# Performance work log

Hardware: AMD Instinct MI355X
Metric: run time of the kernel (lower is better)

Reference implementation:

```python
import jax, jax.numpy as jnp
import numpy as np

B, N, DIM, T, H, DH = 4, 2048, 512, 16, 8, 64
EPS = 1e-5


def setup_inputs() -> dict:
    key = jax.random.key(0)
    ks = jax.random.split(key, 7)
    x = jax.random.normal(ks[0], (B, N, DIM), dtype=jnp.float32)
    # time-distance matrix, e.g. months between scans, in [0, 24)
    R = jax.random.uniform(ks[1], (B, T, T), dtype=jnp.float32) * 24.0
    gamma = jnp.ones((DIM,), dtype=jnp.float32)
    beta = jnp.zeros((DIM,), dtype=jnp.float32)
    W_qkv = jax.random.normal(ks[2], (DIM, 3 * H * DH), dtype=jnp.float32) * 0.02
    W_out = jax.random.normal(ks[3], (H * DH, DIM), dtype=jnp.float32) * 0.02
    a = jax.random.uniform(ks[4], (H,), dtype=jnp.float32)          # torch.rand(heads)
    c = 12.0 * jax.random.uniform(ks[5], (H,), dtype=jnp.float32)   # 12 * torch.rand(heads)
    return {"x": x, "R": R, "gamma": gamma, "beta": beta,
            "W_qkv": W_qkv, "W_out": W_out, "a": a, "c": c}


def reference(x, R, gamma, beta, W_qkv, W_out, a, c):
    b, n, dim = x.shape
    t = R.shape[-1]
    num_patches = n // t
    scale = DH ** -0.5

    # LayerNorm
    mu = jnp.mean(x, axis=-1, keepdims=True)
    var = jnp.mean(jnp.square(x - mu), axis=-1, keepdims=True)
    xn = (x - mu) * jax.lax.rsqrt(var + EPS) * gamma + beta

    # QKV projection -> [b, h, n, d]
    qkv = xn @ W_qkv  # [b, n, 3*h*d]
    q, k, v = jnp.split(qkv, 3, axis=-1)
    def to_heads(z):
        return z.reshape(b, n, H, DH).transpose(0, 2, 1, 3)
    q, k, v = to_heads(q), to_heads(k), to_heads(v)

    # attention scores with ReLU then learned sigmoid time-decay mask
    dots = jnp.einsum('bhnd,bhmd->bhnm', q, k) * scale
    dots = jax.nn.relu(dots)

    # flipped-sigmoid decay: 1 / (1 + exp(|a|*R - |c|)), per head  -> [b, h, t, t]
    decay = 1.0 / (1.0 + jnp.exp(jnp.abs(a)[None, :, None, None] * R[:, None, :, :]
                                 - jnp.abs(c)[None, :, None, None]))
    # expand timepoint mask to token resolution (repeat_interleave on both axes)
    decay = jnp.repeat(jnp.repeat(decay, num_patches, axis=2), num_patches, axis=3)

    attn = jax.nn.softmax(dots * decay, axis=-1)
    out = jnp.einsum('bhnm,bhmd->bhnd', attn, v)
    out = out.transpose(0, 2, 1, 3).reshape(b, n, H * DH)
    return out @ W_out  # dropout is identity at eval
```

## Files before the change

### kernel.cpp

```cpp
#include <hip/hip_runtime.h>
#include <math.h>

#define B_   4
#define N_   2048
#define DIM_ 512
#define T_   16
#define H_   8
#define DH_  64

typedef unsigned short ushort_t;
typedef __attribute__((ext_vector_type(8))) short bf16x8;
typedef __attribute__((ext_vector_type(16))) float f32x16;

__device__ inline ushort_t bf16_rn(float x) {
  unsigned u = __builtin_bit_cast(unsigned, x);
  u += 0x7FFFu + ((u >> 16) & 1u);
  return (ushort_t)(u >> 16);
}
__device__ inline float bf16f(ushort_t h) {
  return __builtin_bit_cast(float, (unsigned)h << 16);
}
__device__ inline unsigned pack2(ushort_t a, ushort_t b) {
  return (unsigned)a | ((unsigned)b << 16);
}
__device__ inline void split2(float x, ushort_t &h, ushort_t &l) {
  h = bf16_rn(x);
  l = bf16_rn(x - bf16f(h));
}
__device__ inline unsigned cvt_pk_bf16(float lo, float hi) {
  unsigned r;
  asm("v_cvt_pk_bf16_f32 %0, %1, %2" : "=v"(r) : "v"(lo), "v"(hi));
  return r;
}
__device__ inline void permlane32_swap(unsigned &x, unsigned &y) {
  asm volatile("v_permlane32_swap_b32 %0, %1" : "+v"(x), "+v"(y));
}
__device__ inline void gload_lds16(const ushort_t* g, ushort_t* l) {
  __builtin_amdgcn_global_load_lds(
      (const __attribute__((address_space(1))) unsigned int*)(g),
      (__attribute__((address_space(3))) unsigned int*)(l),
      16, 0, 0);
}

__global__ __launch_bounds__(256) void prep_kernel(
    const float* __restrict__ x, const float* __restrict__ gamma,
    const float* __restrict__ beta, const float* __restrict__ Wqkv,
    const float* __restrict__ Wout,
    ushort_t* __restrict__ xnh, ushort_t* __restrict__ xnl,
    ushort_t* __restrict__ wqh, ushort_t* __restrict__ wql,
    ushort_t* __restrict__ woh, ushort_t* __restrict__ wol) {
  __shared__ float Ts[64][68];
  int bidx = blockIdx.x;
  int tid = threadIdx.x;
  if (bidx < 256) {
    const float* src; ushort_t* dh; ushort_t* dl; int Nn, n0, k0;
    if (bidx < 192) {
      src = Wqkv; dh = wqh; dl = wql; Nn = 1536;
      n0 = (bidx % 24) * 64; k0 = (bidx / 24) * 64;
    } else {
      int l = bidx - 192;
      src = Wout; dh = woh; dl = wol; Nn = 512;
      n0 = (l % 8) * 64; k0 = (l / 8) * 64;
    }
#pragma unroll
    for (int it = 0; it < 4; ++it) {
      int idx = tid + it * 256;
      int r = idx >> 4, c4 = (idx & 15) * 4;
      *(float4*)&Ts[r][c4] = *(const float4*)&src[(size_t)(k0 + r) * Nn + n0 + c4];
    }
    __syncthreads();
#pragma unroll
    for (int it = 0; it < 2; ++it) {
      int idx = tid + it * 256;
      int n = idx >> 3, kc = (idx & 7) * 8;
      ushort_t hs[8], ls[8];
#pragma unroll
      for (int j = 0; j < 8; ++j) split2(Ts[kc + j][n], hs[j], ls[j]);
      uint4 uh, ul;
      uh.x = pack2(hs[0], hs[1]); uh.y = pack2(hs[2], hs[3]);
      uh.z = pack2(hs[4], hs[5]); uh.w = pack2(hs[6], hs[7]);
      ul.x = pack2(ls[0], ls[1]); ul.y = pack2(ls[2], ls[3]);
      ul.z = pack2(ls[4], ls[5]); ul.w = pack2(ls[6], ls[7]);
      size_t o = (size_t)(n0 + n) * 512 + k0 + kc;
      *(uint4*)&dh[o] = uh;
      *(uint4*)&dl[o] = ul;
    }
  } else {
    int row  = (bidx - 256) * 4 + (tid >> 6);
    int lane = tid & 63;
    const float4* xr = (const float4*)(x + (size_t)row * DIM_);
    float4 v0 = xr[lane * 2 + 0];
    float4 v1 = xr[lane * 2 + 1];
    float s  = v0.x + v0.y + v0.z + v0.w + v1.x + v1.y + v1.z + v1.w;
    float ss = v0.x*v0.x + v0.y*v0.y + v0.z*v0.z + v0.w*v0.w
             + v1.x*v1.x + v1.y*v1.y + v1.z*v1.z + v1.w*v1.w;
#pragma unroll
    for (int off = 32; off > 0; off >>= 1) {
      s  += __shfl_xor(s, off);
      ss += __shfl_xor(ss, off);
    }
    float mu  = s * (1.0f / DIM_);
    float var = ss * (1.0f / DIM_) - mu * mu;
    float rstd = rsqrtf(var + 1e-5f);
    float4 g0 = *(const float4*)&gamma[lane * 8];
    float4 g1 = *(const float4*)&gamma[lane * 8 + 4];
    float4 b0 = *(const float4*)&beta[lane * 8];
    float4 b1 = *(const float4*)&beta[lane * 8 + 4];
    float xv[8] = {v0.x, v0.y, v0.z, v0.w, v1.x, v1.y, v1.z, v1.w};
    float gv[8] = {g0.x, g0.y, g0.z, g0.w, g1.x, g1.y, g1.z, g1.w};
    float bv[8] = {b0.x, b0.y, b0.z, b0.w, b1.x, b1.y, b1.z, b1.w};
    ushort_t hs[8], ls[8];
#pragma unroll
    for (int j = 0; j < 8; ++j) {
      float xn = (xv[j] - mu) * rstd * gv[j] + bv[j];
      split2(xn, hs[j], ls[j]);
    }
    uint4 uh, ul;
    uh.x = pack2(hs[0], hs[1]); uh.y = pack2(hs[2], hs[3]);
    uh.z = pack2(hs[4], hs[5]); uh.w = pack2(hs[6], hs[7]);
    ul.x = pack2(ls[0], ls[1]); ul.y = pack2(ls[2], ls[3]);
    ul.z = pack2(ls[4], ls[5]); ul.w = pack2(ls[6], ls[7]);
    size_t o = (size_t)row * DIM_ + lane * 8;
    *(uint4*)&xnh[o] = uh;
    *(uint4*)&xnl[o] = ul;
  }
}

__global__ __launch_bounds__(256) void qkv_gemm_mfma(
    const ushort_t* __restrict__ xnh, const ushort_t* __restrict__ xnl,
    const ushort_t* __restrict__ wth, const ushort_t* __restrict__ wtl,
    ushort_t* __restrict__ qh, ushort_t* __restrict__ ql,
    ushort_t* __restrict__ kho, ushort_t* __restrict__ klo,
    ushort_t* __restrict__ vt) {
  __shared__ ushort_t Ah[128 * 40], Al[128 * 40], Bh[128 * 40], Bl[128 * 40];
  int tid = threadIdx.x;
  int w = tid >> 6, lane = tid & 63, l31 = lane & 31, g = lane >> 5;
  int wm = w >> 1, wn = w & 1;
  int idx = blockIdx.x;
  int xcd = idx & 7, local = idx >> 3;
  int n0 = (local % 12) * 128;
  int m0 = ((local / 12) * 8 + xcd) * 128;

  f32x16 acc[2][2];
#pragma unroll
  for (int i = 0; i < 2; ++i)
#pragma unroll
    for (int j = 0; j < 2; ++j)
#pragma unroll
      for (int e = 0; e < 16; ++e) acc[i][j][e] = 0.0f;

  int fm[2], fc[2];
#pragma unroll
  for (int it = 0; it < 2; ++it) {
    int f = tid + it * 256;
    fm[it] = f >> 2;
    fc[it] = (f & 3) * 8;
  }

#pragma unroll 1
  for (int kt = 0; kt < 16; ++kt) {
    __syncthreads();
#pragma unroll
    for (int it = 0; it < 2; ++it) {
      size_t ao = (size_t)(m0 + fm[it]) * 512 + kt * 32 + fc[it];
      size_t bo = (size_t)(n0 + fm[it]) * 512 + kt * 32 + fc[it];
      uint4 tah = *(const uint4*)&xnh[ao];
      uint4 tal = *(const uint4*)&xnl[ao];
      uint4 tbh = *(const uint4*)&wth[bo];
      uint4 tbl = *(const uint4*)&wtl[bo];
      int o = fm[it] * 40 + fc[it];
      *(uint4*)&Ah[o] = tah;
      *(uint4*)&Al[o] = tal;
      *(uint4*)&Bh[o] = tbh;
      *(uint4*)&Bl[o] = tbl;
    }
    __syncthreads();
#pragma unroll
    for (int kc = 0; kc < 2; ++kc) {
      int off = kc * 16 + 8 * g;
      bf16x8 afh[2], afl[2], bfh[2], bfl[2];
#pragma unroll
      for (int rb = 0; rb < 2; ++rb) {
        int r = (wm * 64 + rb * 32 + l31) * 40 + off;
        afh[rb] = *(const bf16x8*)&Ah[r];
        afl[rb] = *(const bf16x8*)&Al[r];
      }
#pragma unroll
      for (int cb = 0; cb < 2; ++cb) {
        int r = (wn * 64 + cb * 32 + l31) * 40 + off;
        bfh[cb] = *(const bf16x8*)&Bh[r];
        bfl[cb] = *(const bf16x8*)&Bl[r];
      }
#pragma unroll
      for (int rb = 0; rb < 2; ++rb)
#pragma unroll
        for (int cb = 0; cb < 2; ++cb) {
          acc[rb][cb] = __builtin_amdgcn_mfma_f32_32x32x16_bf16(afh[rb], bfh[cb], acc[rb][cb], 0, 0, 0);
          acc[rb][cb] = __builtin_amdgcn_mfma_f32_32x32x16_bf16(afh[rb], bfl[cb], acc[rb][cb], 0, 0, 0);
          acc[rb][cb] = __builtin_amdgcn_mfma_f32_32x32x16_bf16(afl[rb], bfh[cb], acc[rb][cb], 0, 0, 0);
        }
    }
  }

  int part = n0 >> 9;
#pragma unroll
  for (int rb = 0; rb < 2; ++rb) {
    int m_base = m0 + wm * 64 + rb * 32;
#pragma unroll
    for (int cb = 0; cb < 2; ++cb) {
      int n_g = n0 + wn * 64 + cb * 32 + l31;
      int rem = n_g & 511, hh = rem >> 6, d = rem & 63;
      if (part == 2) {
#pragma unroll
        for (int grp = 0; grp < 4; ++grp) {
          int m_g = m_base + grp * 8 + 4 * g;
          int bb = m_g >> 11, tok = m_g & 2047;
          uint2 pk;
          pk.x = pack2(bf16_rn(acc[rb][cb][grp * 4 + 0]), bf16_rn(acc[rb][cb][grp * 4 + 1]));
          pk.y = pack2(bf16_rn(acc[rb][cb][grp * 4 + 2]), bf16_rn(acc[rb][cb][grp * 4 + 3]));
          *(uint2*)&vt[((size_t)(bb * 8 + hh) * 64 + d) * 2048 + tok] = pk;
        }
      } else {
        float sc = (part == 0) ? 0.125f : 1.0f;
        ushort_t* dsth = (part == 0) ? qh : kho;
        ushort_t* dstl = (part == 0) ? ql : klo;
#pragma unroll
        for (int reg = 0; reg < 16; ++reg) {
          int row = (reg & 3) + 8 * (reg >> 2) + 4 * g;
          int m_g = m_base + row;
          int bb = m_g >> 11, tok = m_g & 2047;
          ushort_t hi, lo;
          split2(acc[rb][cb][reg] * sc, hi, lo);
          size_t addr = ((size_t)(bb * 8 + hh) * 2048 + tok) * 64 + d;
          dsth[addr] = hi;
          dstl[addr] = lo;
        }
      }
    }
  }
}

__global__ __launch_bounds__(256, 2) void attn_mfma(
    const ushort_t* __restrict__ qh, const ushort_t* __restrict__ ql,
    const ushort_t* __restrict__ kho, const ushort_t* __restrict__ klo,
    const ushort_t* __restrict__ vt, const float* __restrict__ R,
    const float* __restrict__ a, const float* __restrict__ c,
    ushort_t* __restrict__ aoh, ushort_t* __restrict__ aol) {
  __shared__ __align__(16) ushort_t KhS[2 * 4608];
  __shared__ __align__(16) ushort_t KlS[2 * 4608];
  __shared__ __align__(16) ushort_t VtS[2 * 4608];
  __shared__ float rsS[128];
  __shared__ float decl2S[16];

  int tid = threadIdx.x;
  int w = tid >> 6, lane = tid & 63, l31 = lane & 31, g = lane >> 5;
  int bh = blockIdx.x;
  int qt = blockIdx.y;
  int b = bh >> 3, h = bh & 7;

  int qrow = qt * 128 + w * 32 + l31;
  size_t qoff = ((size_t)bh * 2048 + qrow) * 64;
  bf16x8 qfh[4], qfl[4];
#pragma unroll
  for (int d0i = 0; d0i < 4; ++d0i) {
    qfh[d0i] = *(const bf16x8*)&qh[qoff + d0i * 16 + 8 * g];
    qfl[d0i] = *(const bf16x8*)&ql[qoff + d0i * 16 + 8 * g];
  }

  const ushort_t* kbase = kho + (size_t)bh * 2048 * 64;
  const ushort_t* lbase = klo + (size_t)bh * 2048 * 64;
  const ushort_t* vbase = vt + (size_t)bh * 64 * 2048;

  if (tid < 16) {
    float aab = fabsf(a[h]);
    float cab = fabsf(c[h]);
    float Rv = R[b * (T_ * T_) + qt * T_ + tid];
    decl2S[tid] = 1.4426950408889634f / (1.0f + __expf(aab * Rv - cab));
  }

  int r_[3], j8_[3];
#pragma unroll
  for (int i = 0; i < 3; ++i) {
    int ch = (i < 2) ? (w + i * 4) : 8;
    int u = ch * 512 + lane * 8;
    int r = u / 72;
    int j = (u - r * 72) >> 3;
    r_[i] = r;
    j8_[i] = (j == 8) ? 0 : (j << 3);
  }
  int a8 = (w < 3) ? w : 0;

  f32x16 oacc[2];
#pragma unroll
  for (int t = 0; t < 2; ++t)
#pragma unroll
    for (int i = 0; i < 16; ++i) oacc[t][i] = 0.0f;
  float rsp[4] = {0.0f, 0.0f, 0.0f, 0.0f};

  {
#pragma unroll
    for (int i = 0; i < 2; ++i) {
      int cb = (w + i * 4) * 512;
      gload_lds16(&kbase[(size_t)r_[i] * 64 + j8_[i]], &KhS[cb]);
      gload_lds16(&lbase[(size_t)r_[i] * 64 + j8_[i]], &KlS[cb]);
      gload_lds16(&vbase[(size_t)r_[i] * 2048 + j8_[i]], &VtS[cb]);
    }
    int cb8 = 8 * 512;
    if (a8 == 0)      gload_lds16(&kbase[(size_t)r_[2] * 64 + j8_[2]], &KhS[cb8]);
    else if (a8 == 1) gload_lds16(&lbase[(size_t)r_[2] * 64 + j8_[2]], &KlS[cb8]);
    else              gload_lds16(&vbase[(size_t)r_[2] * 2048 + j8_[2]], &VtS[cb8]);
  }
  __syncthreads();

  int cur = 0;

#pragma unroll 1
  for (int kt = 0; kt < 32; ++kt) {
    int kb = cur * 4608;

    float decl2 = decl2S[kt >> 1];
    bf16x8 kfh[2][4], kfl[2][4], vf[2][4];
#pragma unroll
    for (int khalf = 0; khalf < 2; ++khalf) {
      int krow = kb + (khalf * 32 + l31) * 72;
#pragma unroll
      for (int d0i = 0; d0i < 4; ++d0i) {
        int off = krow + d0i * 16 + 8 * g;
        kfh[khalf][d0i] = *(const bf16x8*)&KhS[off];
        kfl[khalf][d0i] = *(const bf16x8*)&KlS[off];
      }
    }
#pragma unroll
    for (int dt = 0; dt < 2; ++dt) {
      int vrow = kb + (dt * 32 + l31) * 72;
#pragma unroll
      for (int kc = 0; kc < 4; ++kc)
        vf[dt][kc] = *(const bf16x8*)&VtS[vrow + kc * 16 + 8 * g];
    }
    __builtin_amdgcn_sched_barrier(0);

    if (kt + 1 < 32) {
      int lb = (cur ^ 1) * 4608;
      int kk = kt + 1;
#pragma unroll
      for (int i = 0; i < 2; ++i) {
        int cb = lb + (w + i * 4) * 512;
        gload_lds16(&kbase[(size_t)kk * 4096 + r_[i] * 64 + j8_[i]], &KhS[cb]);
        gload_lds16(&lbase[(size_t)kk * 4096 + r_[i] * 64 + j8_[i]], &KlS[cb]);
        gload_lds16(&vbase[(size_t)r_[i] * 2048 + kk * 64 + j8_[i]], &VtS[cb]);
      }
      int cb8 = lb + 8 * 512;
      if (a8 == 0)      gload_lds16(&kbase[(size_t)kk * 4096 + r_[2] * 64 + j8_[2]], &KhS[cb8]);
      else if (a8 == 1) gload_lds16(&lbase[(size_t)kk * 4096 + r_[2] * 64 + j8_[2]], &KlS[cb8]);
      else              gload_lds16(&vbase[(size_t)r_[2] * 2048 + kk * 64 + j8_[2]], &VtS[cb8]);
    }
    __builtin_amdgcn_sched_barrier(0);

    bf16x8 pa[4];
#pragma unroll
    for (int khalf = 0; khalf < 2; ++khalf) {
      f32x16 sacc;
#pragma unroll
      for (int i = 0; i < 16; ++i) sacc[i] = 0.0f;
#pragma unroll
      for (int d0i = 0; d0i < 4; ++d0i) {
        sacc = __builtin_amdgcn_mfma_f32_32x32x16_bf16(kfh[khalf][d0i], qfh[d0i], sacc, 0, 0, 0);
        sacc = __builtin_amdgcn_mfma_f32_32x32x16_bf16(kfl[khalf][d0i], qfh[d0i], sacc, 0, 0, 0);
        sacc = __builtin_amdgcn_mfma_f32_32x32x16_bf16(kfh[khalf][d0i], qfl[d0i], sacc, 0, 0, 0);
      }
#pragma unroll
      for (int reg = 0; reg < 16; ++reg) {
        float pvv = exp2f(fmaxf(sacc[reg], 0.0f) * decl2);
        rsp[reg & 3] += pvv;
        sacc[reg] = pvv;
      }
#pragma unroll
      for (int hf = 0; hf < 2; ++hf) {
        unsigned d0 = cvt_pk_bf16(sacc[hf * 8 + 0], sacc[hf * 8 + 1]);
        unsigned d1 = cvt_pk_bf16(sacc[hf * 8 + 2], sacc[hf * 8 + 3]);
        unsigned d2 = cvt_pk_bf16(sacc[hf * 8 + 4], sacc[hf * 8 + 5]);
        unsigned d3 = cvt_pk_bf16(sacc[hf * 8 + 6], sacc[hf * 8 + 7]);
        permlane32_swap(d0, d2);
        permlane32_swap(d1, d3);
        uint4 u; u.x = d0; u.y = d1; u.z = d2; u.w = d3;
        pa[khalf * 2 + hf] = __builtin_bit_cast(bf16x8, u);
      }
    }

#pragma unroll
    for (int dt = 0; dt < 2; ++dt)
#pragma unroll
      for (int kc = 0; kc < 4; ++kc)
        oacc[dt] = __builtin_amdgcn_mfma_f32_32x32x16_bf16(pa[kc], vf[dt][kc], oacc[dt], 0, 0, 0);

    __builtin_amdgcn_s_barrier();
    cur ^= 1;
  }

  float rs = (rsp[0] + rsp[1]) + (rsp[2] + rsp[3]);
  rs += __shfl_xor(rs, 32);
  rsS[w * 32 + l31] = rs;

#pragma unroll
  for (int reg = 0; reg < 16; ++reg) {
    int row = (reg & 3) + 8 * (reg >> 2) + 4 * g;
    float invs = 1.0f / rsS[w * 32 + row];
    int tok = qt * 128 + w * 32 + row;
#pragma unroll
    for (int dt = 0; dt < 2; ++dt) {
      int d = dt * 32 + l31;
      ushort_t hi, lo;
      split2(oacc[dt][reg] * invs, hi, lo);
      size_t addr = ((size_t)b * 2048 + tok) * 512 + h * 64 + d;
      aoh[addr] = hi;
      aol[addr] = lo;
    }
  }
}

__global__ __launch_bounds__(256) void out_gemm_mfma(
    const ushort_t* __restrict__ ah, const ushort_t* __restrict__ al,
    const ushort_t* __restrict__ wth, const ushort_t* __restrict__ wtl,
    float* __restrict__ out) {
  __shared__ ushort_t Ah[128 * 40], Al[128 * 40], Bh[128 * 40], Bl[128 * 40];
  int tid = threadIdx.x;
  int w = tid >> 6, lane = tid & 63, l31 = lane & 31, g = lane >> 5;
  int wm = w >> 1, wn = w & 1;
  int idx = blockIdx.x;
  int xcd = idx & 7, local = idx >> 3;
  int n0 = (local & 3) * 128;
  int m0 = ((local >> 2) * 8 + xcd) * 128;

  f32x16 acc[2][2];
#pragma unroll
  for (int i = 0; i < 2; ++i)
#pragma unroll
    for (int j = 0; j < 2; ++j)
#pragma unroll
      for (int e = 0; e < 16; ++e) acc[i][j][e] = 0.0f;

  int fm[2], fc[2];
#pragma unroll
  for (int it = 0; it < 2; ++it) {
    int f = tid + it * 256;
    fm[it] = f >> 2;
    fc[it] = (f & 3) * 8;
  }

#pragma unroll 1
  for (int kt = 0; kt < 16; ++kt) {
    __syncthreads();
#pragma unroll
    for (int it = 0; it < 2; ++it) {
      size_t ao = (size_t)(m0 + fm[it]) * 512 + kt * 32 + fc[it];
      size_t bo = (size_t)(n0 + fm[it]) * 512 + kt * 32 + fc[it];
      uint4 tah = *(const uint4*)&ah[ao];
      uint4 tal = *(const uint4*)&al[ao];
      uint4 tbh = *(const uint4*)&wth[bo];
      uint4 tbl = *(const uint4*)&wtl[bo];
      int o = fm[it] * 40 + fc[it];
      *(uint4*)&Ah[o] = tah;
      *(uint4*)&Al[o] = tal;
      *(uint4*)&Bh[o] = tbh;
      *(uint4*)&Bl[o] = tbl;
    }
    __syncthreads();
#pragma unroll
    for (int kc = 0; kc < 2; ++kc) {
      int off = kc * 16 + 8 * g;
      bf16x8 afh[2], afl[2], bfh[2], bfl[2];
#pragma unroll
      for (int rb = 0; rb < 2; ++rb) {
        int r = (wm * 64 + rb * 32 + l31) * 40 + off;
        afh[rb] = *(const bf16x8*)&Ah[r];
        afl[rb] = *(const bf16x8*)&Al[r];
      }
#pragma unroll
      for (int cb = 0; cb < 2; ++cb) {
        int r = (wn * 64 + cb * 32 + l31) * 40 + off;
        bfh[cb] = *(const bf16x8*)&Bh[r];
        bfl[cb] = *(const bf16x8*)&Bl[r];
      }
#pragma unroll
      for (int rb = 0; rb < 2; ++rb)
#pragma unroll
        for (int cb = 0; cb < 2; ++cb) {
          acc[rb][cb] = __builtin_amdgcn_mfma_f32_32x32x16_bf16(afh[rb], bfh[cb], acc[rb][cb], 0, 0, 0);
          acc[rb][cb] = __builtin_amdgcn_mfma_f32_32x32x16_bf16(afh[rb], bfl[cb], acc[rb][cb], 0, 0, 0);
          acc[rb][cb] = __builtin_amdgcn_mfma_f32_32x32x16_bf16(afl[rb], bfh[cb], acc[rb][cb], 0, 0, 0);
        }
    }
  }

#pragma unroll
  for (int rb = 0; rb < 2; ++rb) {
    int m_base = m0 + wm * 64 + rb * 32;
#pragma unroll
    for (int cb = 0; cb < 2; ++cb) {
      int n_g = n0 + wn * 64 + cb * 32 + l31;
#pragma unroll
      for (int reg = 0; reg < 16; ++reg) {
        int row = (reg & 3) + 8 * (reg >> 2) + 4 * g;
        out[(size_t)(m_base + row) * 512 + n_g] = acc[rb][cb][reg];
      }
    }
  }
}

extern "C" void kernel_launch(void* const* d_in, const int* in_sizes, int n_in,
                              void* d_out, int out_size, void* d_ws, size_t ws_size,
                              hipStream_t stream) {
  (void)in_sizes; (void)n_in;
  const float* x     = (const float*)d_in[0];
  const float* R     = (const float*)d_in[1];
  const float* gamma = (const float*)d_in[2];
  const float* beta  = (const float*)d_in[3];
  const float* Wqkv  = (const float*)d_in[4];
  const float* Wout  = (const float*)d_in[5];
  const float* av    = (const float*)d_in[6];
  const float* cv    = (const float*)d_in[7];
  float* out = (float*)d_out;

  const size_t EL  = (size_t)B_ * N_ * DIM_;
  const size_t SZT = EL * sizeof(ushort_t);

  char* p = (char*)d_ws;
  ushort_t* wqh = (ushort_t*)p;                  p += (size_t)1536 * 512 * 2;
  ushort_t* wql = (ushort_t*)p;                  p += (size_t)1536 * 512 * 2;
  ushort_t* woh = (ushort_t*)p;                  p += (size_t)512 * 512 * 2;
  ushort_t* wol = (ushort_t*)p;                  p += (size_t)512 * 512 * 2;
  ushort_t* qhb = (ushort_t*)p;                  p += SZT;
  ushort_t* qlb = (ushort_t*)p;                  p += SZT;
  ushort_t* khb = (ushort_t*)p;                  p += SZT;
  ushort_t* klb = (ushort_t*)p;                  p += SZT;
  ushort_t* vtb = (ushort_t*)p;                  p += SZT;
  size_t base_need = (size_t)(p - (char*)d_ws);
  size_t needA = base_need + 2 * SZT;

  bool planA = (ws_size >= needA);
  ushort_t* xnh = planA ? (ushort_t*)p : (ushort_t*)d_out;
  ushort_t* xnl = xnh + EL;
  float* gemm_dst = planA ? out : (float*)qhb;

  prep_kernel<<<dim3(2304), dim3(256), 0, stream>>>(x, gamma, beta, Wqkv, Wout,
                                                    xnh, xnl, wqh, wql, woh, wol);
  qkv_gemm_mfma<<<dim3(768), dim3(256), 0, stream>>>(xnh, xnl, wqh, wql,
                                                     qhb, qlb, khb, klb, vtb);
  attn_mfma<<<dim3(32, 16), dim3(256), 0, stream>>>(qhb, qlb, khb, klb, vtb,
                                                    R, av, cv, xnh, xnl);
  out_gemm_mfma<<<dim3(256), dim3(256), 0, stream>>>(xnh, xnl, woh, wol, gemm_dst);
  if (!planA) {
    hipMemcpyAsync(out, gemm_dst, (size_t)out_size * sizeof(float),
                   hipMemcpyDeviceToDevice, stream);
  }
}
```

Measured before the change: 235.6 us.

## Shrink attention blocks to two waves with single-buffered LDS and priority hints

The attention kernel now uses 128-thread blocks covering 64 query rows, doubling the grid, and single-buffers the K/Kl/Vt tiles in LDS instead of double-buffering them. This cuts LDS per block so more blocks can be resident. The price is that each K/V tile is reloaded by twice as many blocks, and the loop needs extra waits and barriers, which removes the load/compute overlap within a block. It also raises wave priority around the MFMA sections and replaces exp2f with raw v_exp_f32 to cut softmax instruction overhead.

```diff
diff --git a/kernel.cpp b/kernel.cpp
--- a/kernel.cpp
+++ b/kernel.cpp
@@ -34,6 +34,11 @@
 }
 __device__ inline void permlane32_swap(unsigned &x, unsigned &y) {
   asm volatile("v_permlane32_swap_b32 %0, %1" : "+v"(x), "+v"(y));
+}
+__device__ inline float exp2_raw(float x) {
+  float r;
+  asm("v_exp_f32 %0, %1" : "=v"(r) : "v"(x));
+  return r;
 }
 __device__ inline void gload_lds16(const ushort_t* g, ushort_t* l) {
   __builtin_amdgcn_global_load_lds(
@@ -240,16 +245,16 @@
   }
 }
 
-__global__ __launch_bounds__(256, 2) void attn_mfma(
+__global__ __launch_bounds__(128, 2) void attn_mfma(
     const ushort_t* __restrict__ qh, const ushort_t* __restrict__ ql,
     const ushort_t* __restrict__ kho, const ushort_t* __restrict__ klo,
     const ushort_t* __restrict__ vt, const float* __restrict__ R,
     const float* __restrict__ a, const float* __restrict__ c,
     ushort_t* __restrict__ aoh, ushort_t* __restrict__ aol) {
-  __shared__ __align__(16) ushort_t KhS[2 * 4608];
-  __shared__ __align__(16) ushort_t KlS[2 * 4608];
-  __shared__ __align__(16) ushort_t VtS[2 * 4608];
-  __shared__ float rsS[128];
+  __shared__ __align__(16) ushort_t KhS[4608];
+  __shared__ __align__(16) ushort_t KlS[4608];
+  __shared__ __align__(16) ushort_t VtS[4608];
+  __shared__ float rsS[64];
   __shared__ float decl2S[16];
 
   int tid = threadIdx.x;
@@ -258,7 +263,7 @@
   int qt = blockIdx.y;
   int b = bh >> 3, h = bh & 7;
 
-  int qrow = qt * 128 + w * 32 + l31;
+  int qrow = qt * 64 + w * 32 + l31;
   size_t qoff = ((size_t)bh * 2048 + qrow) * 64;
   bf16x8 qfh[4], qfl[4];
 #pragma unroll
@@ -274,21 +279,23 @@
   if (tid < 16) {
     float aab = fabsf(a[h]);
     float cab = fabsf(c[h]);
-    float Rv = R[b * (T_ * T_) + qt * T_ + tid];
+    float Rv = R[b * (T_ * T_) + (qt >> 1) * T_ + tid];
     decl2S[tid] = 1.4426950408889634f / (1.0f + __expf(aab * Rv - cab));
   }
 
-  int r_[3], j8_[3];
-#pragma unroll
-  for (int i = 0; i < 3; ++i) {
-    int ch = (i < 2) ? (w + i * 4) : 8;
-    int u = ch * 512 + lane * 8;
+  int r_[4], j8_[4];
+#pragma unroll
+  for (int i = 0; i < 4; ++i) {
+    int u = (w * 4 + i) * 512 + lane * 8;
     int r = u / 72;
     int j = (u - r * 72) >> 3;
     r_[i] = r;
     j8_[i] = (j == 8) ? 0 : (j << 3);
   }
-  int a8 = (w < 3) ? w : 0;
+  int u8 = 8 * 512 + lane * 8;
+  int r8 = u8 / 72;
+  int j8v = (u8 - r8 * 72) >> 3;
+  int j88 = (j8v == 8) ? 0 : (j8v << 3);
 
   f32x16 oacc[2];
 #pragma unroll
@@ -299,30 +306,28 @@
 
   {
 #pragma unroll
-    for (int i = 0; i < 2; ++i) {
-      int cb = (w + i * 4) * 512;
+    for (int i = 0; i < 4; ++i) {
+      int cb = (w * 4 + i) * 512;
       gload_lds16(&kbase[(size_t)r_[i] * 64 + j8_[i]], &KhS[cb]);
       gload_lds16(&lbase[(size_t)r_[i] * 64 + j8_[i]], &KlS[cb]);
       gload_lds16(&vbase[(size_t)r_[i] * 2048 + j8_[i]], &VtS[cb]);
     }
-    int cb8 = 8 * 512;
-    if (a8 == 0)      gload_lds16(&kbase[(size_t)r_[2] * 64 + j8_[2]], &KhS[cb8]);
-    else if (a8 == 1) gload_lds16(&lbase[(size_t)r_[2] * 64 + j8_[2]], &KlS[cb8]);
-    else              gload_lds16(&vbase[(size_t)r_[2] * 2048 + j8_[2]], &VtS[cb8]);
+    if (w == 0) {
+      gload_lds16(&kbase[(size_t)r8 * 64 + j88], &KhS[8 * 512]);
+      gload_lds16(&lbase[(size_t)r8 * 64 + j88], &KlS[8 * 512]);
+    } else {
+      gload_lds16(&vbase[(size_t)r8 * 2048 + j88], &VtS[8 * 512]);
+    }
   }
   __syncthreads();
-
-  int cur = 0;
 
 #pragma unroll 1
   for (int kt = 0; kt < 32; ++kt) {
-    int kb = cur * 4608;
-
     float decl2 = decl2S[kt >> 1];
     bf16x8 kfh[2][4], kfl[2][4], vf[2][4];
 #pragma unroll
     for (int khalf = 0; khalf < 2; ++khalf) {
-      int krow = kb + (khalf * 32 + l31) * 72;
+      int krow = (khalf * 32 + l31) * 72;
 #pragma unroll
       for (int d0i = 0; d0i < 4; ++d0i) {
         int off = krow + d0i * 16 + 8 * g;
@@ -332,27 +337,30 @@
     }
 #pragma unroll
     for (int dt = 0; dt < 2; ++dt) {
-      int vrow = kb + (dt * 32 + l31) * 72;
+      int vrow = (dt * 32 + l31) * 72;
 #pragma unroll
       for (int kc = 0; kc < 4; ++kc)
         vf[dt][kc] = *(const bf16x8*)&VtS[vrow + kc * 16 + 8 * g];
     }
+    asm volatile("s_waitcnt lgkmcnt(0)" ::: "memory");
     __builtin_amdgcn_sched_barrier(0);
+    __builtin_amdgcn_s_barrier();
 
     if (kt + 1 < 32) {
-      int lb = (cur ^ 1) * 4608;
       int kk = kt + 1;
 #pragma unroll
-      for (int i = 0; i < 2; ++i) {
-        int cb = lb + (w + i * 4) * 512;
+      for (int i = 0; i < 4; ++i) {
+        int cb = (w * 4 + i) * 512;
         gload_lds16(&kbase[(size_t)kk * 4096 + r_[i] * 64 + j8_[i]], &KhS[cb]);
         gload_lds16(&lbase[(size_t)kk * 4096 + r_[i] * 64 + j8_[i]], &KlS[cb]);
         gload_lds16(&vbase[(size_t)r_[i] * 2048 + kk * 64 + j8_[i]], &VtS[cb]);
       }
-      int cb8 = lb + 8 * 512;
-      if (a8 == 0)      gload_lds16(&kbase[(size_t)kk * 4096 + r_[2] * 64 + j8_[2]], &KhS[cb8]);
-      else if (a8 == 1) gload_lds16(&lbase[(size_t)kk * 4096 + r_[2] * 64 + j8_[2]], &KlS[cb8]);
-      else              gload_lds16(&vbase[(size_t)r_[2] * 2048 + kk * 64 + j8_[2]], &VtS[cb8]);
+      if (w == 0) {
+        gload_lds16(&kbase[(size_t)kk * 4096 + r8 * 64 + j88], &KhS[8 * 512]);
+        gload_lds16(&lbase[(size_t)kk * 4096 + r8 * 64 + j88], &KlS[8 * 512]);
+      } else {
+        gload_lds16(&vbase[(size_t)r8 * 2048 + kk * 64 + j88], &VtS[8 * 512]);
+      }
     }
     __builtin_amdgcn_sched_barrier(0);
 
@@ -362,15 +370,17 @@
       f32x16 sacc;
 #pragma unroll
       for (int i = 0; i < 16; ++i) sacc[i] = 0.0f;
+      __builtin_amdgcn_s_setprio(1);
 #pragma unroll
       for (int d0i = 0; d0i < 4; ++d0i) {
         sacc = __builtin_amdgcn_mfma_f32_32x32x16_bf16(kfh[khalf][d0i], qfh[d0i], sacc, 0, 0, 0);
         sacc = __builtin_amdgcn_mfma_f32_32x32x16_bf16(kfl[khalf][d0i], qfh[d0i], sacc, 0, 0, 0);
         sacc = __builtin_amdgcn_mfma_f32_32x32x16_bf16(kfh[khalf][d0i], qfl[d0i], sacc, 0, 0, 0);
       }
+      __builtin_amdgcn_s_setprio(0);
 #pragma unroll
       for (int reg = 0; reg < 16; ++reg) {
-        float pvv = exp2f(fmaxf(sacc[reg], 0.0f) * decl2);
+        float pvv = exp2_raw(fmaxf(sacc[reg], 0.0f) * decl2);
         rsp[reg & 3] += pvv;
         sacc[reg] = pvv;
       }
@@ -387,14 +397,16 @@
       }
     }
 
+    __builtin_amdgcn_s_setprio(1);
 #pragma unroll
     for (int dt = 0; dt < 2; ++dt)
 #pragma unroll
       for (int kc = 0; kc < 4; ++kc)
         oacc[dt] = __builtin_amdgcn_mfma_f32_32x32x16_bf16(pa[kc], vf[dt][kc], oacc[dt], 0, 0, 0);
-
+    __builtin_amdgcn_s_setprio(0);
+
+    asm volatile("s_waitcnt vmcnt(0)" ::: "memory");
     __builtin_amdgcn_s_barrier();
-    cur ^= 1;
   }
 
   float rs = (rsp[0] + rsp[1]) + (rsp[2] + rsp[3]);
@@ -405,7 +417,7 @@
   for (int reg = 0; reg < 16; ++reg) {
     int row = (reg & 3) + 8 * (reg >> 2) + 4 * g;
     float invs = 1.0f / rsS[w * 32 + row];
-    int tok = qt * 128 + w * 32 + row;
+    int tok = qt * 64 + w * 32 + row;
 #pragma unroll
     for (int dt = 0; dt < 2; ++dt) {
       int d = dt * 32 + l31;
@@ -546,7 +558,7 @@
                                                     xnh, xnl, wqh, wql, woh, wol);
   qkv_gemm_mfma<<<dim3(768), dim3(256), 0, stream>>>(xnh, xnl, wqh, wql,
                                                      qhb, qlb, khb, klb, vtb);
-  attn_mfma<<<dim3(32, 16), dim3(256), 0, stream>>>(qhb, qlb, khb, klb, vtb,
+  attn_mfma<<<dim3(32, 32), dim3(128), 0, stream>>>(qhb, qlb, khb, klb, vtb,
                                                     R, av, cv, xnh, xnl);
   out_gemm_mfma<<<dim3(256), dim3(256), 0, stream>>>(xnh, xnl, woh, wol, gemm_dst);
   if (!planA) {
```

Result: slower. 241.6 us (+2.6%).

## Load GEMM tiles via direct global-to-LDS loads, use raw v_exp in attention

Applied to the files above, without the earlier changes.

Both projection GEMMs now stage their tiles with global_load_lds instead of register round-trips. Each wave fills one of the four hi/lo operand tiles, and the padding column is filled with a duplicate chunk so the padded 40-element row stride is kept. The attention softmax uses the raw v_exp_f32 instruction instead of exp2f, which avoids range-handling code. An explicit vmcnt(0) wait is added before the attention loop barrier to order the async LDS loads. The aim is to save VGPR traffic and instructions in tile staging. The cost is that only one wave issues loads per tile and the waits are coarse.

```diff
diff --git a/kernel.cpp b/kernel.cpp
--- a/kernel.cpp
+++ b/kernel.cpp
@@ -34,6 +34,11 @@
 }
 __device__ inline void permlane32_swap(unsigned &x, unsigned &y) {
   asm volatile("v_permlane32_swap_b32 %0, %1" : "+v"(x), "+v"(y));
+}
+__device__ inline float exp2_raw(float x) {
+  float r;
+  asm("v_exp_f32 %0, %1" : "=v"(r) : "v"(x));
+  return r;
 }
 __device__ inline void gload_lds16(const ushort_t* g, ushort_t* l) {
   __builtin_amdgcn_global_load_lds(
@@ -132,7 +137,10 @@
     ushort_t* __restrict__ qh, ushort_t* __restrict__ ql,
     ushort_t* __restrict__ kho, ushort_t* __restrict__ klo,
     ushort_t* __restrict__ vt) {
-  __shared__ ushort_t Ah[128 * 40], Al[128 * 40], Bh[128 * 40], Bl[128 * 40];
+  __shared__ __align__(16) ushort_t Ah[128 * 40];
+  __shared__ __align__(16) ushort_t Al[128 * 40];
+  __shared__ __align__(16) ushort_t Bh[128 * 40];
+  __shared__ __align__(16) ushort_t Bl[128 * 40];
   int tid = threadIdx.x;
   int w = tid >> 6, lane = tid & 63, l31 = lane & 31, g = lane >> 5;
   int wm = w >> 1, wn = w & 1;
@@ -149,30 +157,35 @@
 #pragma unroll
       for (int e = 0; e < 16; ++e) acc[i][j][e] = 0.0f;
 
-  int fm[2], fc[2];
-#pragma unroll
-  for (int it = 0; it < 2; ++it) {
-    int f = tid + it * 256;
-    fm[it] = f >> 2;
-    fc[it] = (f & 3) * 8;
+  int rowbase = (w < 2) ? m0 : n0;
+  int off_[10];
+#pragma unroll
+  for (int ci = 0; ci < 10; ++ci) {
+    int u = ci * 512 + lane * 8;
+    int r = u / 40;
+    int j = (u - r * 40) >> 3;
+    off_[ci] = (rowbase + r) * 512 + ((j == 4) ? 0 : (j << 3));
   }
 
 #pragma unroll 1
   for (int kt = 0; kt < 16; ++kt) {
     __syncthreads();
-#pragma unroll
-    for (int it = 0; it < 2; ++it) {
-      size_t ao = (size_t)(m0 + fm[it]) * 512 + kt * 32 + fc[it];
-      size_t bo = (size_t)(n0 + fm[it]) * 512 + kt * 32 + fc[it];
-      uint4 tah = *(const uint4*)&xnh[ao];
-      uint4 tal = *(const uint4*)&xnl[ao];
-      uint4 tbh = *(const uint4*)&wth[bo];
-      uint4 tbl = *(const uint4*)&wtl[bo];
-      int o = fm[it] * 40 + fc[it];
-      *(uint4*)&Ah[o] = tah;
-      *(uint4*)&Al[o] = tal;
-      *(uint4*)&Bh[o] = tbh;
-      *(uint4*)&Bl[o] = tbl;
+    if (w == 0) {
+#pragma unroll
+      for (int ci = 0; ci < 10; ++ci)
+        gload_lds16(&xnh[(size_t)off_[ci] + kt * 32], &Ah[ci * 512]);
+    } else if (w == 1) {
+#pragma unroll
+      for (int ci = 0; ci < 10; ++ci)
+        gload_lds16(&xnl[(size_t)off_[ci] + kt * 32], &Al[ci * 512]);
+    } else if (w == 2) {
+#pragma unroll
+      for (int ci = 0; ci < 10; ++ci)
+        gload_lds16(&wth[(size_t)off_[ci] + kt * 32], &Bh[ci * 512]);
+    } else {
+#pragma unroll
+      for (int ci = 0; ci < 10; ++ci)
+        gload_lds16(&wtl[(size_t)off_[ci] + kt * 32], &Bl[ci * 512]);
     }
     __syncthreads();
 #pragma unroll
@@ -370,7 +383,7 @@
       }
 #pragma unroll
       for (int reg = 0; reg < 16; ++reg) {
-        float pvv = exp2f(fmaxf(sacc[reg], 0.0f) * decl2);
+        float pvv = exp2_raw(fmaxf(sacc[reg], 0.0f) * decl2);
         rsp[reg & 3] += pvv;
         sacc[reg] = pvv;
       }
@@ -393,6 +406,7 @@
       for (int kc = 0; kc < 4; ++kc)
         oacc[dt] = __builtin_amdgcn_mfma_f32_32x32x16_bf16(pa[kc], vf[dt][kc], oacc[dt], 0, 0, 0);
 
+    asm volatile("s_waitcnt vmcnt(0)" ::: "memory");
     __builtin_amdgcn_s_barrier();
     cur ^= 1;
   }
@@ -422,7 +436,10 @@
     const ushort_t* __restrict__ ah, const ushort_t* __restrict__ al,
     const ushort_t* __restrict__ wth, const ushort_t* __restrict__ wtl,
     float* __restrict__ out) {
-  __shared__ ushort_t Ah[128 * 40], Al[128 * 40], Bh[128 * 40], Bl[128 * 40];
+  __shared__ __align__(16) ushort_t Ah[128 * 40];
+  __shared__ __align__(16) ushort_t Al[128 * 40];
+  __shared__ __align__(16) ushort_t Bh[128 * 40];
+  __shared__ __align__(16) ushort_t Bl[128 * 40];
   int tid = threadIdx.x;
   int w = tid >> 6, lane = tid & 63, l31 = lane & 31, g = lane >> 5;
   int wm = w >> 1, wn = w & 1;
@@ -439,30 +456,35 @@
 #pragma unroll
       for (int e = 0; e < 16; ++e) acc[i][j][e] = 0.0f;
 
-  int fm[2], fc[2];
-#pragma unroll
-  for (int it = 0; it < 2; ++it) {
-    int f = tid + it * 256;
-    fm[it] = f >> 2;
-    fc[it] = (f & 3) * 8;
+  int rowbase = (w < 2) ? m0 : n0;
+  int off_[10];
+#pragma unroll
+  for (int ci = 0; ci < 10; ++ci) {
+    int u = ci * 512 + lane * 8;
+    int r = u / 40;
+    int j = (u - r * 40) >> 3;
+    off_[ci] = (rowbase + r) * 512 + ((j == 4) ? 0 : (j << 3));
   }
 
 #pragma unroll 1
   for (int kt = 0; kt < 16; ++kt) {
     __syncthreads();
-#pragma unroll
-    for (int it = 0; it < 2; ++it) {
-      size_t ao = (size_t)(m0 + fm[it]) * 512 + kt * 32 + fc[it];
-      size_t bo = (size_t)(n0 + fm[it]) * 512 + kt * 32 + fc[it];
-      uint4 tah = *(const uint4*)&ah[ao];
-      uint4 tal = *(const uint4*)&al[ao];
-      uint4 tbh = *(const uint4*)&wth[bo];
-      uint4 tbl = *(const uint4*)&wtl[bo];
-      int o = fm[it] * 40 + fc[it];
-      *(uint4*)&Ah[o] = tah;
-      *(uint4*)&Al[o] = tal;
-      *(uint4*)&Bh[o] = tbh;
-      *(uint4*)&Bl[o] = tbl;
+    if (w == 0) {
+#pragma unroll
+      for (int ci = 0; ci < 10; ++ci)
+        gload_lds16(&ah[(size_t)off_[ci] + kt * 32], &Ah[ci * 512]);
+    } else if (w == 1) {
+#pragma unroll
+      for (int ci = 0; ci < 10; ++ci)
+        gload_lds16(&al[(size_t)off_[ci] + kt * 32], &Al[ci * 512]);
+    } else if (w == 2) {
+#pragma unroll
+      for (int ci = 0; ci < 10; ++ci)
+        gload_lds16(&wth[(size_t)off_[ci] + kt * 32], &Bh[ci * 512]);
+    } else {
+#pragma unroll
+      for (int ci = 0; ci < 10; ++ci)
+        gload_lds16(&wtl[(size_t)off_[ci] + kt * 32], &Bl[ci * 512]);
     }
     __syncthreads();
 #pragma unroll
```

Result: faster. 229.0 us (-2.8%).
